# Performance work log

Hardware: AMD Instinct MI355X
Metric: run time of the kernel (lower is better)

Reference implementation:

```python
import jax, jax.numpy as jnp
import numpy as np

IN_CH = 1024
HID_CH = 1024
NUM_HEADS = 16
HEAD_DIM = HID_CH // NUM_HEADS
SCALE = (HID_CH / NUM_HEADS) ** (-0.25)


def _xavier(key, shape):
    fan_out, fan_in = shape
    limit = np.sqrt(6.0 / (fan_in + fan_out)).astype(np.float32)
    return jax.random.uniform(key, shape, jnp.float32, -limit, limit)


def setup_inputs() -> dict:
    key = jax.random.key(0)
    ks = jax.random.split(key, 5)
    B, T, L = 4, 2048, 512
    inpt = jax.random.normal(ks[0], (B, IN_CH, T), jnp.float32)
    aux = jax.random.normal(ks[1], (L, IN_CH), jnp.float32)
    q_w = _xavier(ks[2], (HID_CH, IN_CH))
    q_b = jnp.zeros((HID_CH,), jnp.float32)
    kv_w = _xavier(ks[3], (2 * HID_CH, IN_CH))
    kv_b = jnp.zeros((2 * HID_CH,), jnp.float32)
    out_w = _xavier(ks[4], (IN_CH, HID_CH))
    out_b = jnp.zeros((IN_CH,), jnp.float32)
    return {"inpt": inpt, "aux": aux, "q_w": q_w, "q_b": q_b,
            "kv_w": kv_w, "kv_b": kv_b, "out_w": out_w, "out_b": out_b}


def reference(inpt, aux, q_w, q_b, kv_w, kv_b, out_w, out_b):
    # inpt: (B, C, T), aux: (L, C)
    B, C, T = inpt.shape
    x = jnp.swapaxes(inpt, -2, -1)                     # (B, T, C)
    q = (x @ q_w.T + q_b) * SCALE                      # (B, T, H*D)
    kv = aux @ kv_w.T + kv_b                           # (L, 2*H*D)
    k, v = jnp.split(kv, 2, axis=-1)
    k = k * SCALE
    q = q.reshape(B, T, NUM_HEADS, HEAD_DIM)           # (B, T, h, d)
    L = aux.shape[0]
    k = k.reshape(L, NUM_HEADS, HEAD_DIM)              # (L, h, d)
    v = v.reshape(L, NUM_HEADS, HEAD_DIM)
    e = jnp.einsum('bihd,jhd->bijh', q, k)             # (B, T, L, h)
    attn = jax.nn.softmax(e, axis=2)                   # softmax over key axis j
    out = jnp.einsum('bijh,jhd->bihd', attn, v)        # (B, T, h, d)
    out = out.reshape(B, T, HID_CH) @ out_w.T + out_b  # (B, T, C)
    return inpt + jnp.swapaxes(out, -2, -1)            # (B, C, T)
```

## Files before the change

kernel.cpp:

```cpp
#include <hip/hip_runtime.h>
#include <cstdint>
#include <cstddef>

typedef __bf16 bf16;
typedef __bf16 bf16x4 __attribute__((ext_vector_type(4)));
typedef __bf16 bf16x8 __attribute__((ext_vector_type(8)));
typedef float f32x4 __attribute__((ext_vector_type(4)));

static constexpr float SCALE_F = 0.35355339059327373f;

#define AS1 __attribute__((address_space(1)))
#define AS3 __attribute__((address_space(3)))

__device__ __forceinline__ void load_lds16(const void* g, void* l) {
  __builtin_amdgcn_global_load_lds((AS1 void*)g, (AS3 void*)l, 16, 0, 0);
}


__global__ void cvt_f32_bf16(const float* __restrict__ in, bf16* __restrict__ out, int n4) {
  int i = blockIdx.x * blockDim.x + threadIdx.x;
  if (i >= n4) return;
  float4 v = reinterpret_cast<const float4*>(in)[i];
  bf16x4 o;
  o[0] = (bf16)v.x; o[1] = (bf16)v.y; o[2] = (bf16)v.z; o[3] = (bf16)v.w;
  reinterpret_cast<bf16x4*>(out)[i] = o;
}

__global__ void transpose_in(const float* __restrict__ inpt, bf16* __restrict__ X) {
  __shared__ float tile[32][33];
  int b = blockIdx.z;
  int t0 = blockIdx.x * 32, c0 = blockIdx.y * 32;
  int tx = threadIdx.x, ty = threadIdx.y;
  const float* src = inpt + ((size_t)b * 1024 + c0) * 2048 + t0;
#pragma unroll
  for (int i = 0; i < 4; ++i) tile[ty + i * 8][tx] = src[(size_t)(ty + i * 8) * 2048 + tx];
  __syncthreads();
  bf16* dst = X + ((size_t)b * 2048 + t0) * 1024 + c0;
#pragma unroll
  for (int i = 0; i < 4; ++i) dst[(size_t)(ty + i * 8) * 1024 + tx] = (bf16)tile[tx][ty + i * 8];
}

__global__ void residual_out(const float* __restrict__ inpt, const bf16* __restrict__ Z,
                             float* __restrict__ out) {
  __shared__ float tile[32][33];
  int b = blockIdx.z;
  int t0 = blockIdx.x * 32, c0 = blockIdx.y * 32;
  int tx = threadIdx.x, ty = threadIdx.y;
  const bf16* zsrc = Z + ((size_t)b * 2048 + t0) * 1024 + c0;
#pragma unroll
  for (int i = 0; i < 4; ++i) tile[ty + i * 8][tx] = (float)zsrc[(size_t)(ty + i * 8) * 1024 + tx];
  __syncthreads();
  size_t ob = ((size_t)b * 1024 + c0) * 2048 + t0;
#pragma unroll
  for (int i = 0; i < 4; ++i) {
    size_t idx = ob + (size_t)(ty + i * 8) * 2048 + tx;
    out[idx] = inpt[idx] + tile[tx][ty + i * 8];
  }
}

template <int MODE>
__global__ __launch_bounds__(256, 2) void gemm_bt(const bf16* __restrict__ A,
                                                  const bf16* __restrict__ Bw,
                                                  const float* __restrict__ bias,
                                                  bf16* __restrict__ out0,
                                                  bf16* __restrict__ out1, int M, int N, int K) {
  __shared__ __align__(16) char sA[16384];
  __shared__ __align__(16) char sB[16384];
  const int tid = threadIdx.x;
  const int lane = tid & 63;
  const int wave = tid >> 6;
  const int wm = wave >> 1, wn = wave & 1;
  const int m0 = blockIdx.x * 128, n0 = blockIdx.y * 128;
  f32x4 acc[4][4] = {};

  for (int kt = 0; kt < K; kt += 64) {
#pragma unroll
    for (int j = 0; j < 4; ++j) {
      int i = tid + j * 256;
      int r = i >> 3, q = i & 7;
      int so = (q ^ (r & 7)) << 4;
      load_lds16((const char*)(A + (size_t)(m0 + r) * K + kt) + so, sA + (size_t)i * 16);
      load_lds16((const char*)(Bw + (size_t)(n0 + r) * K + kt) + so, sB + (size_t)i * 16);
    }
    asm volatile("s_waitcnt vmcnt(0)" ::: "memory");
    __syncthreads();
    bf16x8 af[4][2], bfr[4][2];
#pragma unroll
    for (int mi = 0; mi < 4; ++mi)
#pragma unroll
      for (int kk = 0; kk < 2; ++kk) {
        int rr = wm * 64 + mi * 16 + (lane & 15);
        int w = kk * 64 + ((lane >> 4) << 4);
        af[mi][kk] = *(const bf16x8*)(sA + (size_t)rr * 128 + (w ^ ((rr & 7) << 4)));
        int r2 = wn * 64 + mi * 16 + (lane & 15);
        bfr[mi][kk] = *(const bf16x8*)(sB + (size_t)r2 * 128 + (w ^ ((r2 & 7) << 4)));
      }
#pragma unroll
    for (int kk = 0; kk < 2; ++kk)
#pragma unroll
      for (int mi = 0; mi < 4; ++mi)
#pragma unroll
        for (int ni = 0; ni < 4; ++ni)
          acc[mi][ni] =
              __builtin_amdgcn_mfma_f32_16x16x32_bf16(af[mi][kk], bfr[ni][kk], acc[mi][ni], 0, 0, 0);
    __syncthreads();
  }

  float bs[4];
#pragma unroll
  for (int ni = 0; ni < 4; ++ni) bs[ni] = bias[n0 + wn * 64 + ni * 16 + (lane & 15)];

#pragma unroll
  for (int mi = 0; mi < 4; ++mi)
#pragma unroll
    for (int ni = 0; ni < 4; ++ni)
#pragma unroll
      for (int j = 0; j < 4; ++j) {
        int row = wm * 64 + mi * 16 + ((lane >> 4) << 2) + j;
        int col = wn * 64 + ni * 16 + (lane & 15);
        int m = m0 + row, n = n0 + col;
        float val = acc[mi][ni][j] + bs[ni];
        if constexpr (MODE == 0) {
          val *= SCALE_F;
          int bb = m >> 11, t = m & 2047, hh = n >> 6, d = n & 63;
          out0[(((size_t)(bb * 16 + hh) * 2048 + t) << 6) + d] = (bf16)val;
        } else if constexpr (MODE == 1) {
          if (n < 1024) {
            int hh = n >> 6, d = n & 63;
            out0[(((size_t)hh * 512 + m) << 6) + d] = (bf16)(val * SCALE_F);
          } else {
            int n2 = n - 1024;
            int hh = n2 >> 6, d = n2 & 63;
            out1[(((size_t)hh * 64 + d) << 9) + m] = (bf16)val;
          }
        } else {
          out0[(size_t)m * 1024 + n] = (bf16)val;
        }
      }
}

__global__ __launch_bounds__(512, 4) void attn_kernel(const bf16* __restrict__ Q,
                                                      const bf16* __restrict__ Kw,
                                                      const bf16* __restrict__ Vt,
                                                      bf16* __restrict__ Y) {
  __shared__ __align__(16) char lds[73728];
  const int tid = threadIdx.x;
  const int lane = tid & 63;
  const int wv = tid >> 6;
  const int g = lane >> 4;
  const int lr = lane & 15;
  const int t0 = blockIdx.x * 64;
  const int bh = blockIdx.y;
  const int b = bh >> 4, h = bh & 15;

  {
    const bf16* Qh = Q + ((size_t)(b * 16 + h) * 2048 + t0) * 64;
    int r = tid >> 3, c = tid & 7;
    load_lds16((const char*)Qh + r * 128 + ((c * 16) ^ ((r & 7) << 4)),
               lds + 65536 + (size_t)tid * 16);
  }
  asm volatile("s_waitcnt vmcnt(0)" ::: "memory");
  __syncthreads();

  f32x4 acc[4][4] = {};
  const bf16* Kh = Kw + (size_t)h * 512 * 64;
#pragma unroll
  for (int kk = 0; kk < 2; ++kk) {
    bf16x8 ka[4], qb[4];
#pragma unroll
    for (int mi = 0; mi < 4; ++mi) {
      int key = wv * 64 + mi * 16 + lr;
      ka[mi] = *(const bf16x8*)((const char*)Kh + (size_t)key * 128 + kk * 64 + g * 16);
    }
#pragma unroll
    for (int ni = 0; ni < 4; ++ni) {
      int q = ni * 16 + lr;
      qb[ni] = *(const bf16x8*)(lds + 65536 + (size_t)q * 128 +
                                ((kk * 64 + g * 16) ^ ((q & 7) << 4)));
    }
#pragma unroll
    for (int mi = 0; mi < 4; ++mi)
#pragma unroll
      for (int ni = 0; ni < 4; ++ni)
        acc[mi][ni] =
            __builtin_amdgcn_mfma_f32_16x16x32_bf16(ka[mi], qb[ni], acc[mi][ni], 0, 0, 0);
  }

#pragma unroll
  for (int mi = 0; mi < 4; ++mi)
#pragma unroll
    for (int ni = 0; ni < 4; ++ni) {
      int q = ni * 16 + lr;
      bf16x4 w;
#pragma unroll
      for (int j = 0; j < 4; ++j) w[j] = (bf16)__expf(acc[mi][ni][j] - 16.0f);
      int byt = (wv * 128 + mi * 32 + g * 8) ^ ((q & 7) << 4);
      *(bf16x4*)(lds + (size_t)q * 1024 + byt) = w;
    }
  __syncthreads();

  const int mi_o = wv >> 1;
  const int n0 = (wv & 1) * 2;
  const bf16* Vh = Vt + (size_t)h * 64 * 512;
  const bf16 one = (bf16)1.0f;
  const bf16x8 ones = {one, one, one, one, one, one, one, one};
  f32x4 o0 = {}, o1 = {}, s0 = {}, s1 = {};
  const int d = mi_o * 16 + lr;
  const int q0 = n0 * 16 + lr, q1 = q0 + 16;
#pragma unroll
  for (int kk = 0; kk < 16; ++kk) {
    bf16x8 va = *(const bf16x8*)((const char*)Vh + (size_t)d * 1024 + kk * 64 + g * 16);
    bf16x8 p0 = *(const bf16x8*)(lds + (size_t)q0 * 1024 + ((kk * 64 + g * 16) ^ ((q0 & 7) << 4)));
    bf16x8 p1 = *(const bf16x8*)(lds + (size_t)q1 * 1024 + ((kk * 64 + g * 16) ^ ((q1 & 7) << 4)));
    o0 = __builtin_amdgcn_mfma_f32_16x16x32_bf16(va, p0, o0, 0, 0, 0);
    o1 = __builtin_amdgcn_mfma_f32_16x16x32_bf16(va, p1, o1, 0, 0, 0);
    s0 = __builtin_amdgcn_mfma_f32_16x16x32_bf16(ones, p0, s0, 0, 0, 0);
    s1 = __builtin_amdgcn_mfma_f32_16x16x32_bf16(ones, p1, s1, 0, 0, 0);
  }
  __syncthreads();

  {
    float i0 = 1.0f / s0[0], i1 = 1.0f / s1[0];
    int byt = mi_o * 64 + g * 16;
    f32x4 w0, w1;
#pragma unroll
    for (int j = 0; j < 4; ++j) {
      w0[j] = o0[j] * i0;
      w1[j] = o1[j] * i1;
    }
    *(f32x4*)(lds + (size_t)q0 * 256 + (byt ^ ((q0 & 7) << 4))) = w0;
    *(f32x4*)(lds + (size_t)q1 * 256 + (byt ^ ((q1 & 7) << 4))) = w1;
  }
  __syncthreads();

  {
    int q = tid >> 3, sub = tid & 7;
    int base = sub * 32;
    f32x4 a = *(const f32x4*)(lds + (size_t)q * 256 + (base ^ ((q & 7) << 4)));
    f32x4 c = *(const f32x4*)(lds + (size_t)q * 256 + ((base + 16) ^ ((q & 7) << 4)));
    bf16x8 w;
#pragma unroll
    for (int j = 0; j < 4; ++j) {
      w[j] = (bf16)a[j];
      w[4 + j] = (bf16)c[j];
    }
    *(bf16x8*)((char*)Y + (((size_t)(b * 2048 + t0 + q) * 1024 + h * 64 + sub * 8) * 2)) = w;
  }
}


extern "C" void kernel_launch(void* const* d_in, const int* in_sizes, int n_in, void* d_out,
                              int out_size, void* d_ws, size_t ws_size, hipStream_t stream) {
  const float* inpt = (const float*)d_in[0];
  const float* aux = (const float*)d_in[1];
  const float* q_w = (const float*)d_in[2];
  const float* q_b = (const float*)d_in[3];
  const float* kv_w = (const float*)d_in[4];
  const float* kv_b = (const float*)d_in[5];
  const float* out_w = (const float*)d_in[6];
  const float* out_b = (const float*)d_in[7];
  float* out = (float*)d_out;
  char* ws = (char*)d_ws;
  bf16* X = (bf16*)(ws + 0);
  bf16* QZ = (bf16*)(ws + (16u << 20));
  bf16* qwb = (bf16*)(ws + (32u << 20));
  bf16* kvwb = (bf16*)(ws + (34u << 20));
  bf16* owb = (bf16*)(ws + (38u << 20));
  bf16* auxb = (bf16*)(ws + (40u << 20));
  bf16* Kws = (bf16*)(ws + (41u << 20));
  bf16* Vtw = (bf16*)(ws + (42u << 20));

  cvt_f32_bf16<<<1024, 256, 0, stream>>>(q_w, qwb, 1024 * 1024 / 4);
  cvt_f32_bf16<<<2048, 256, 0, stream>>>(kv_w, kvwb, 2048 * 1024 / 4);
  cvt_f32_bf16<<<1024, 256, 0, stream>>>(out_w, owb, 1024 * 1024 / 4);
  cvt_f32_bf16<<<512, 256, 0, stream>>>(aux, auxb, 512 * 1024 / 4);
  transpose_in<<<dim3(64, 32, 4), dim3(32, 8), 0, stream>>>(inpt, X);

  gemm_bt<1><<<dim3(4, 16), 256, 0, stream>>>(auxb, kvwb, kv_b, Kws, Vtw, 512, 2048, 1024);
  gemm_bt<0><<<dim3(64, 8), 256, 0, stream>>>(X, qwb, q_b, QZ, nullptr, 8192, 1024, 1024);
  attn_kernel<<<dim3(32, 64), 512, 0, stream>>>(QZ, Kws, Vtw, X );
  gemm_bt<2><<<dim3(64, 8), 256, 0, stream>>>(X, owb, out_b, QZ , nullptr, 8192,
                                              1024, 1024);
  residual_out<<<dim3(64, 32, 4), dim3(32, 8), 0, stream>>>(inpt, QZ, out);
}
```

Measured before the change: 238.3 us.

## Merge launches, fuse Q/KV GEMMs, compute softmax sums via shuffles in attention

The four weight-conversion launches become one kernel, and the Q-projection and KV-projection GEMMs become a single launch that dispatches on block index. In attention, K and V fragments are preloaded into registers, the QK product is done per query column, and softmax row sums come from register accumulation plus cross-lane shuffles and a small LDS reduction instead of extra MFMA work with a ones matrix. This removes launch overhead and redundant MFMAs, at the cost of more registers (and possible occupancy loss) and more LDS.

```diff
diff --git a/kernel.cpp b/kernel.cpp
--- a/kernel.cpp
+++ b/kernel.cpp
@@ -17,13 +17,22 @@
 }
 
 
-__global__ void cvt_f32_bf16(const float* __restrict__ in, bf16* __restrict__ out, int n4) {
+__global__ void cvt_all(const float* __restrict__ a, bf16* __restrict__ oa,
+                        const float* __restrict__ b, bf16* __restrict__ ob,
+                        const float* __restrict__ c, bf16* __restrict__ oc,
+                        const float* __restrict__ d, bf16* __restrict__ od) {
   int i = blockIdx.x * blockDim.x + threadIdx.x;
-  if (i >= n4) return;
-  float4 v = reinterpret_cast<const float4*>(in)[i];
+  const float* src;
+  bf16* dst;
+  int off;
+  if (i < 262144) { src = a; dst = oa; off = i; }
+  else if (i < 786432) { src = b; dst = ob; off = i - 262144; }
+  else if (i < 1048576) { src = c; dst = oc; off = i - 786432; }
+  else { src = d; dst = od; off = i - 1048576; }
+  float4 v = reinterpret_cast<const float4*>(src)[off];
   bf16x4 o;
   o[0] = (bf16)v.x; o[1] = (bf16)v.y; o[2] = (bf16)v.z; o[3] = (bf16)v.w;
-  reinterpret_cast<bf16x4*>(out)[i] = o;
+  reinterpret_cast<bf16x4*>(dst)[off] = o;
 }
 
 __global__ void transpose_in(const float* __restrict__ inpt, bf16* __restrict__ X) {
@@ -58,12 +67,100 @@
   }
 }
 
-template <int MODE>
-__global__ __launch_bounds__(256, 2) void gemm_bt(const bf16* __restrict__ A,
-                                                  const bf16* __restrict__ Bw,
-                                                  const float* __restrict__ bias,
-                                                  bf16* __restrict__ out0,
-                                                  bf16* __restrict__ out1, int M, int N, int K) {
+
+__global__ __launch_bounds__(256, 2) void gemm_qkv(
+    const bf16* __restrict__ X, const bf16* __restrict__ qwb, const float* __restrict__ q_b,
+    bf16* __restrict__ Qout, const bf16* __restrict__ auxb, const bf16* __restrict__ kvwb,
+    const float* __restrict__ kv_b, bf16* __restrict__ Kout, bf16* __restrict__ Vout) {
+  __shared__ __align__(16) char sA[16384];
+  __shared__ __align__(16) char sB[16384];
+  const int tid = threadIdx.x;
+  const int lane = tid & 63;
+  const int wave = tid >> 6;
+  const int wm = wave >> 1, wn = wave & 1;
+  const int bid = blockIdx.x;
+  const bool isQ = bid < 512;
+  const bf16 *A, *Bw;
+  const float* bias;
+  int m0, n0;
+  if (isQ) {
+    A = X; Bw = qwb; bias = q_b;
+    m0 = (bid >> 3) * 128; n0 = (bid & 7) * 128;
+  } else {
+    int b2 = bid - 512;
+    A = auxb; Bw = kvwb; bias = kv_b;
+    m0 = (b2 & 3) * 128; n0 = (b2 >> 2) * 128;
+  }
+  f32x4 acc[4][4] = {};
+
+  for (int kt = 0; kt < 1024; kt += 64) {
+#pragma unroll
+    for (int j = 0; j < 4; ++j) {
+      int i = tid + j * 256;
+      int r = i >> 3, q = i & 7;
+      int so = (q ^ (r & 7)) << 4;
+      load_lds16((const char*)(A + (size_t)(m0 + r) * 1024 + kt) + so, sA + (size_t)i * 16);
+      load_lds16((const char*)(Bw + (size_t)(n0 + r) * 1024 + kt) + so, sB + (size_t)i * 16);
+    }
+    asm volatile("s_waitcnt vmcnt(0)" ::: "memory");
+    __syncthreads();
+    bf16x8 af[4][2], bfr[4][2];
+#pragma unroll
+    for (int mi = 0; mi < 4; ++mi)
+#pragma unroll
+      for (int kk = 0; kk < 2; ++kk) {
+        int rr = wm * 64 + mi * 16 + (lane & 15);
+        int w = kk * 64 + ((lane >> 4) << 4);
+        af[mi][kk] = *(const bf16x8*)(sA + (size_t)rr * 128 + (w ^ ((rr & 7) << 4)));
+        int r2 = wn * 64 + mi * 16 + (lane & 15);
+        bfr[mi][kk] = *(const bf16x8*)(sB + (size_t)r2 * 128 + (w ^ ((r2 & 7) << 4)));
+      }
+#pragma unroll
+    for (int kk = 0; kk < 2; ++kk)
+#pragma unroll
+      for (int mi = 0; mi < 4; ++mi)
+#pragma unroll
+        for (int ni = 0; ni < 4; ++ni)
+          acc[mi][ni] =
+              __builtin_amdgcn_mfma_f32_16x16x32_bf16(af[mi][kk], bfr[ni][kk], acc[mi][ni], 0, 0, 0);
+    __syncthreads();
+  }
+
+  float bs[4];
+#pragma unroll
+  for (int ni = 0; ni < 4; ++ni) bs[ni] = bias[n0 + wn * 64 + ni * 16 + (lane & 15)];
+
+#pragma unroll
+  for (int mi = 0; mi < 4; ++mi)
+#pragma unroll
+    for (int ni = 0; ni < 4; ++ni)
+#pragma unroll
+      for (int j = 0; j < 4; ++j) {
+        int row = wm * 64 + mi * 16 + ((lane >> 4) << 2) + j;
+        int col = wn * 64 + ni * 16 + (lane & 15);
+        int m = m0 + row, n = n0 + col;
+        float val = acc[mi][ni][j] + bs[ni];
+        if (isQ) {
+          val *= SCALE_F;
+          int bb = m >> 11, t = m & 2047, hh = n >> 6, d = n & 63;
+          Qout[(((size_t)(bb * 16 + hh) * 2048 + t) << 6) + d] = (bf16)val;
+        } else {
+          if (n < 1024) {
+            int hh = n >> 6, d = n & 63;
+            Kout[(((size_t)hh * 512 + m) << 6) + d] = (bf16)(val * SCALE_F);
+          } else {
+            int n2 = n - 1024;
+            int hh = n2 >> 6, d = n2 & 63;
+            Vout[(((size_t)hh * 64 + d) << 9) + m] = (bf16)val;
+          }
+        }
+      }
+}
+
+__global__ __launch_bounds__(256, 2) void gemm_out(const bf16* __restrict__ A,
+                                                   const bf16* __restrict__ Bw,
+                                                   const float* __restrict__ bias,
+                                                   bf16* __restrict__ out0) {
   __shared__ __align__(16) char sA[16384];
   __shared__ __align__(16) char sB[16384];
   const int tid = threadIdx.x;
@@ -73,14 +170,14 @@
   const int m0 = blockIdx.x * 128, n0 = blockIdx.y * 128;
   f32x4 acc[4][4] = {};
 
-  for (int kt = 0; kt < K; kt += 64) {
+  for (int kt = 0; kt < 1024; kt += 64) {
 #pragma unroll
     for (int j = 0; j < 4; ++j) {
       int i = tid + j * 256;
       int r = i >> 3, q = i & 7;
       int so = (q ^ (r & 7)) << 4;
-      load_lds16((const char*)(A + (size_t)(m0 + r) * K + kt) + so, sA + (size_t)i * 16);
-      load_lds16((const char*)(Bw + (size_t)(n0 + r) * K + kt) + so, sB + (size_t)i * 16);
+      load_lds16((const char*)(A + (size_t)(m0 + r) * 1024 + kt) + so, sA + (size_t)i * 16);
+      load_lds16((const char*)(Bw + (size_t)(n0 + r) * 1024 + kt) + so, sB + (size_t)i * 16);
     }
     asm volatile("s_waitcnt vmcnt(0)" ::: "memory");
     __syncthreads();
@@ -109,7 +206,6 @@
   float bs[4];
 #pragma unroll
   for (int ni = 0; ni < 4; ++ni) bs[ni] = bias[n0 + wn * 64 + ni * 16 + (lane & 15)];
-
 #pragma unroll
   for (int mi = 0; mi < 4; ++mi)
 #pragma unroll
@@ -118,24 +214,7 @@
       for (int j = 0; j < 4; ++j) {
         int row = wm * 64 + mi * 16 + ((lane >> 4) << 2) + j;
         int col = wn * 64 + ni * 16 + (lane & 15);
-        int m = m0 + row, n = n0 + col;
-        float val = acc[mi][ni][j] + bs[ni];
-        if constexpr (MODE == 0) {
-          val *= SCALE_F;
-          int bb = m >> 11, t = m & 2047, hh = n >> 6, d = n & 63;
-          out0[(((size_t)(bb * 16 + hh) * 2048 + t) << 6) + d] = (bf16)val;
-        } else if constexpr (MODE == 1) {
-          if (n < 1024) {
-            int hh = n >> 6, d = n & 63;
-            out0[(((size_t)hh * 512 + m) << 6) + d] = (bf16)(val * SCALE_F);
-          } else {
-            int n2 = n - 1024;
-            int hh = n2 >> 6, d = n2 & 63;
-            out1[(((size_t)hh * 64 + d) << 9) + m] = (bf16)val;
-          }
-        } else {
-          out0[(size_t)m * 1024 + n] = (bf16)val;
-        }
+        out0[(size_t)(m0 + row) * 1024 + n0 + col] = (bf16)(acc[mi][ni][j] + bs[ni]);
       }
 }
 
@@ -143,7 +222,7 @@
                                                       const bf16* __restrict__ Kw,
                                                       const bf16* __restrict__ Vt,
                                                       bf16* __restrict__ Y) {
-  __shared__ __align__(16) char lds[73728];
+  __shared__ __align__(16) char lds[75776];
   const int tid = threadIdx.x;
   const int lane = tid & 63;
   const int wv = tid >> 6;
@@ -153,6 +232,16 @@
   const int bh = blockIdx.y;
   const int b = bh >> 4, h = bh & 15;
 
+  const bf16* Kh = Kw + (size_t)h * 512 * 64;
+  bf16x8 ka[2][4];
+#pragma unroll
+  for (int kk = 0; kk < 2; ++kk)
+#pragma unroll
+    for (int mi = 0; mi < 4; ++mi) {
+      int key = wv * 64 + mi * 16 + lr;
+      ka[kk][mi] = *(const bf16x8*)((const char*)Kh + (size_t)key * 128 + kk * 64 + g * 16);
+    }
+
   {
     const bf16* Qh = Q + ((size_t)(b * 16 + h) * 2048 + t0) * 64;
     int r = tid >> 3, c = tid & 7;
@@ -162,65 +251,70 @@
   asm volatile("s_waitcnt vmcnt(0)" ::: "memory");
   __syncthreads();
 
-  f32x4 acc[4][4] = {};
-  const bf16* Kh = Kw + (size_t)h * 512 * 64;
-#pragma unroll
-  for (int kk = 0; kk < 2; ++kk) {
-    bf16x8 ka[4], qb[4];
+  float psum[4];
+#pragma unroll
+  for (int ni = 0; ni < 4; ++ni) {
+    int q = ni * 16 + lr;
+    f32x4 acc[4] = {};
+#pragma unroll
+    for (int kk = 0; kk < 2; ++kk) {
+      bf16x8 qb = *(const bf16x8*)(lds + 65536 + (size_t)q * 128 +
+                                   ((kk * 64 + g * 16) ^ ((q & 7) << 4)));
+#pragma unroll
+      for (int mi = 0; mi < 4; ++mi)
+        acc[mi] = __builtin_amdgcn_mfma_f32_16x16x32_bf16(ka[kk][mi], qb, acc[mi], 0, 0, 0);
+    }
+    float ps = 0.f;
 #pragma unroll
     for (int mi = 0; mi < 4; ++mi) {
-      int key = wv * 64 + mi * 16 + lr;
-      ka[mi] = *(const bf16x8*)((const char*)Kh + (size_t)key * 128 + kk * 64 + g * 16);
-    }
-#pragma unroll
-    for (int ni = 0; ni < 4; ++ni) {
-      int q = ni * 16 + lr;
-      qb[ni] = *(const bf16x8*)(lds + 65536 + (size_t)q * 128 +
-                                ((kk * 64 + g * 16) ^ ((q & 7) << 4)));
-    }
-#pragma unroll
-    for (int mi = 0; mi < 4; ++mi)
-#pragma unroll
-      for (int ni = 0; ni < 4; ++ni)
-        acc[mi][ni] =
-            __builtin_amdgcn_mfma_f32_16x16x32_bf16(ka[mi], qb[ni], acc[mi][ni], 0, 0, 0);
-  }
-
-#pragma unroll
-  for (int mi = 0; mi < 4; ++mi)
-#pragma unroll
-    for (int ni = 0; ni < 4; ++ni) {
-      int q = ni * 16 + lr;
       bf16x4 w;
 #pragma unroll
-      for (int j = 0; j < 4; ++j) w[j] = (bf16)__expf(acc[mi][ni][j] - 16.0f);
-      int byt = (wv * 128 + mi * 32 + g * 8) ^ ((q & 7) << 4);
-      *(bf16x4*)(lds + (size_t)q * 1024 + byt) = w;
-    }
-  __syncthreads();
-
+      for (int j = 0; j < 4; ++j) {
+        float p = __expf(acc[mi][j] - 16.0f);
+        ps += p;
+        w[j] = (bf16)p;
+      }
+      *(bf16x4*)(lds + (size_t)q * 1024 + ((wv * 128 + mi * 32 + g * 8) ^ ((q & 7) << 4))) = w;
+    }
+    ps += __shfl_xor(ps, 16);
+    ps += __shfl_xor(ps, 32);
+    psum[ni] = ps;
+  }
+  if (lane < 16) {
+#pragma unroll
+    for (int ni = 0; ni < 4; ++ni)
+      *(float*)(lds + 73728 + (((ni * 16 + lr) * 8 + wv) << 2)) = psum[ni];
+  }
+
+  const bf16* Vh = Vt + (size_t)h * 64 * 512;
   const int mi_o = wv >> 1;
-  const int n0 = (wv & 1) * 2;
-  const bf16* Vh = Vt + (size_t)h * 64 * 512;
-  const bf16 one = (bf16)1.0f;
-  const bf16x8 ones = {one, one, one, one, one, one, one, one};
-  f32x4 o0 = {}, o1 = {}, s0 = {}, s1 = {};
   const int d = mi_o * 16 + lr;
-  const int q0 = n0 * 16 + lr, q1 = q0 + 16;
+  bf16x8 va[16];
+#pragma unroll
+  for (int kk = 0; kk < 16; ++kk)
+    va[kk] = *(const bf16x8*)((const char*)Vh + (size_t)d * 1024 + kk * 64 + g * 16);
+  __syncthreads();
+
+  const int q0 = (wv & 1) * 32 + lr, q1 = q0 + 16;
+  f32x4 o0 = {}, o1 = {};
 #pragma unroll
   for (int kk = 0; kk < 16; ++kk) {
-    bf16x8 va = *(const bf16x8*)((const char*)Vh + (size_t)d * 1024 + kk * 64 + g * 16);
     bf16x8 p0 = *(const bf16x8*)(lds + (size_t)q0 * 1024 + ((kk * 64 + g * 16) ^ ((q0 & 7) << 4)));
     bf16x8 p1 = *(const bf16x8*)(lds + (size_t)q1 * 1024 + ((kk * 64 + g * 16) ^ ((q1 & 7) << 4)));
-    o0 = __builtin_amdgcn_mfma_f32_16x16x32_bf16(va, p0, o0, 0, 0, 0);
-    o1 = __builtin_amdgcn_mfma_f32_16x16x32_bf16(va, p1, o1, 0, 0, 0);
-    s0 = __builtin_amdgcn_mfma_f32_16x16x32_bf16(ones, p0, s0, 0, 0, 0);
-    s1 = __builtin_amdgcn_mfma_f32_16x16x32_bf16(ones, p1, s1, 0, 0, 0);
-  }
-  __syncthreads();
+    o0 = __builtin_amdgcn_mfma_f32_16x16x32_bf16(va[kk], p0, o0, 0, 0, 0);
+    o1 = __builtin_amdgcn_mfma_f32_16x16x32_bf16(va[kk], p1, o1, 0, 0, 0);
+  }
+  __syncthreads();
+
+  f32x4 sa0 = *(const f32x4*)(lds + 73728 + q0 * 32);
+  f32x4 sb0 = *(const f32x4*)(lds + 73728 + q0 * 32 + 16);
+  f32x4 sa1 = *(const f32x4*)(lds + 73728 + q1 * 32);
+  f32x4 sb1 = *(const f32x4*)(lds + 73728 + q1 * 32 + 16);
+  float s0v = ((sa0[0] + sa0[1]) + (sa0[2] + sa0[3])) + ((sb0[0] + sb0[1]) + (sb0[2] + sb0[3]));
+  float s1v = ((sa1[0] + sa1[1]) + (sa1[2] + sa1[3])) + ((sb1[0] + sb1[1]) + (sb1[2] + sb1[3]));
 
   {
-    float i0 = 1.0f / s0[0], i1 = 1.0f / s1[0];
+    float i0 = 1.0f / s0v, i1 = 1.0f / s1v;
     int byt = mi_o * 64 + g * 16;
     f32x4 w0, w1;
 #pragma unroll
@@ -270,16 +364,11 @@
   bf16* Kws = (bf16*)(ws + (41u << 20));
   bf16* Vtw = (bf16*)(ws + (42u << 20));
 
-  cvt_f32_bf16<<<1024, 256, 0, stream>>>(q_w, qwb, 1024 * 1024 / 4);
-  cvt_f32_bf16<<<2048, 256, 0, stream>>>(kv_w, kvwb, 2048 * 1024 / 4);
-  cvt_f32_bf16<<<1024, 256, 0, stream>>>(out_w, owb, 1024 * 1024 / 4);
-  cvt_f32_bf16<<<512, 256, 0, stream>>>(aux, auxb, 512 * 1024 / 4);
+  cvt_all<<<4608, 256, 0, stream>>>(q_w, qwb, kv_w, kvwb, out_w, owb, aux, auxb);
   transpose_in<<<dim3(64, 32, 4), dim3(32, 8), 0, stream>>>(inpt, X);
 
-  gemm_bt<1><<<dim3(4, 16), 256, 0, stream>>>(auxb, kvwb, kv_b, Kws, Vtw, 512, 2048, 1024);
-  gemm_bt<0><<<dim3(64, 8), 256, 0, stream>>>(X, qwb, q_b, QZ, nullptr, 8192, 1024, 1024);
+  gemm_qkv<<<576, 256, 0, stream>>>(X, qwb, q_b, QZ, auxb, kvwb, kv_b, Kws, Vtw);
   attn_kernel<<<dim3(32, 64), 512, 0, stream>>>(QZ, Kws, Vtw, X );
-  gemm_bt<2><<<dim3(64, 8), 256, 0, stream>>>(X, owb, out_b, QZ , nullptr, 8192,
-                                              1024, 1024);
+  gemm_out<<<dim3(64, 8), 256, 0, stream>>>(X, owb, out_b, QZ );
   residual_out<<<dim3(64, 32, 4), dim3(32, 8), 0, stream>>>(inpt, QZ, out);
 }
```

Result: faster. 222.7 us (-6.5%).
